# Performance work log

Hardware: AMD Instinct MI355X
Metric: run time of the kernel (lower is better)

The kernel has to match this reference:

```python
import jax, jax.numpy as jnp
import numpy as np

N = 50000
IN_DIM = 512
HID = 64
E = 800000


def setup_inputs() -> dict:
    key = jax.random.key(0)
    k1, k2, k3, k4 = jax.random.split(key, 4)
    x = jax.random.normal(k1, (N, IN_DIM), dtype=jnp.float32)
    edge_index = jax.random.randint(k2, (2, E), 0, N, dtype=jnp.int32)
    # Glorot-ish init for linear weights
    W1 = jax.random.normal(k3, (IN_DIM, HID), dtype=jnp.float32) / np.sqrt(IN_DIM)
    b1 = jnp.zeros((HID,), dtype=jnp.float32)
    W2 = jax.random.normal(k4, (HID, HID), dtype=jnp.float32) / np.sqrt(HID)
    b2 = jnp.zeros((HID,), dtype=jnp.float32)
    return {"x": x, "edge_index": edge_index, "W1": W1, "b1": b1, "W2": W2, "b2": b2}


def gcn_conv(x, src, dst, norm, W, b, n):
    # x' = D^{-1/2} (A+I) D^{-1/2} x W + b  (PyG GCNConv with self-loops)
    h = x @ W                                  # [N, out] dense GEMM
    msg = h[src] * norm[:, None]               # gather + scale per edge
    out = jax.ops.segment_sum(msg, dst, num_segments=n)  # scatter-add
    return out + b


def reference(x, edge_index, W1, b1, W2, b2):
    n = x.shape[0]
    loop = jnp.arange(n, dtype=edge_index.dtype)
    src = jnp.concatenate([edge_index[0], loop])  # add self-loops
    dst = jnp.concatenate([edge_index[1], loop])
    deg = jax.ops.segment_sum(jnp.ones_like(src, dtype=x.dtype), dst, num_segments=n)
    dinv = jnp.where(deg > 0, jax.lax.rsqrt(deg), 0.0)
    norm = dinv[src] * dinv[dst]               # symmetric normalization per edge
    h = gcn_conv(x, src, dst, norm, W1, b1, n)
    h = jax.nn.relu(h)
    # dropout is identity in eval mode (reference baseline)
    z = gcn_conv(h, src, dst, norm, W2, b2, n)
    return z
```

## Files before the change

kernel.cpp:

```cpp
#include <hip/hip_runtime.h>
#include <stdint.h>


typedef __attribute__((ext_vector_type(8))) short short8;
typedef __attribute__((ext_vector_type(4))) float f32x4;

#define SLOTS 64

__device__ __forceinline__ uint32_t bf16_rne(float f) {
  uint32_t u = __float_as_uint(f);
  return (u + 0x7FFFu + ((u >> 16) & 1u)) >> 16;
}

__global__ __launch_bounds__(256) void fill_wfrag_kernel(
    const int* __restrict__ src, const int* __restrict__ dst, int E,
    int* __restrict__ cursor, int* __restrict__ meta,
    const float* __restrict__ W1, const float* __restrict__ W2,
    short8* __restrict__ wh1, short8* __restrict__ wl1,
    short8* __restrict__ wh2, short8* __restrict__ wl2,
    int K1, int K2, int wblocks) {
  if ((int)blockIdx.x >= wblocks) {
    int i = (blockIdx.x - wblocks) * 256 + threadIdx.x;
    if (i < E) {
      int s = __builtin_nontemporal_load(src + i);
      int d = __builtin_nontemporal_load(dst + i);
      int pos = atomicAdd(&cursor[d], 1);
      if (pos < SLOTS) meta[(size_t)d * SLOTS + pos] = s;
    }
    return;
  }
  int idx = blockIdx.x * 256 + threadIdx.x;
  int tot1 = (K1 >> 5) * 256;
  int tot2 = (K2 >> 5) * 256;
  const float* W;
  short8 *wh, *wl;
  if (idx < tot1) {
    W = W1; wh = wh1; wl = wl1;
  } else if (idx < tot1 + tot2) {
    idx -= tot1;
    W = W2; wh = wh2; wl = wl2;
  } else {
    return;
  }
  int lane = idx & 63;
  int ct = (idx >> 6) & 3;
  int kt = idx >> 8;
  int m = lane & 15, q = lane >> 4;
  int col = ct * 16 + m;
  short8 h, l;
#pragma unroll
  for (int j = 0; j < 8; ++j) {
    float f = W[(size_t)(kt * 32 + q * 8 + j) * 64 + col];
    uint32_t hb = bf16_rne(f);
    float hf = __uint_as_float(hb << 16);
    float lo = f - hf;
    h[j] = (short)hb;
    l[j] = (short)bf16_rne(lo);
  }
  wh[idx] = h;
  wl[idx] = l;
}

__global__ __launch_bounds__(256) void gemm_mfma_kernel(
    const float* __restrict__ A, const short8* __restrict__ wh,
    const short8* __restrict__ wl, ushort* __restrict__ outb, int n, int K,
    int gblocks, const int* __restrict__ cursor, float* __restrict__ dinv,
    int ndinv) {
  if ((int)blockIdx.x >= gblocks) {
    int i = (blockIdx.x - gblocks) * 256 + threadIdx.x;
    if (i < ndinv) dinv[i] = rsqrtf((float)(cursor[i] + 1));
    return;
  }
  const int t = threadIdx.x;
  const int lane = t & 63;
  const int m = lane & 15, q = lane >> 4;
  const int row0 = blockIdx.x * 64 + (t >> 6) * 16;
  int r0 = row0 + m;
  if (r0 >= n) r0 = n - 1;
  const float* ap = A + (size_t)r0 * K + q * 8;
  const short8* whp = wh + lane;
  const short8* wlp = wl + lane;
  const int nkt = K >> 5;
  f32x4 acc[4];
#pragma unroll
  for (int c = 0; c < 4; ++c) acc[c] = 0.f;

  f32x4 xa0 = __builtin_nontemporal_load((const f32x4*)ap);
  f32x4 xa1 = __builtin_nontemporal_load((const f32x4*)(ap + 4));
  short8 bh[4] = {whp[0], whp[64], whp[128], whp[192]};
  short8 bl[4] = {wlp[0], wlp[64], wlp[128], wlp[192]};

  auto cvt = [&](const f32x4& u0, const f32x4& u1, short8& hi, short8& lo) {
    float xf[8] = {u0[0], u0[1], u0[2], u0[3], u1[0], u1[1], u1[2], u1[3]};
#pragma unroll
    for (int j = 0; j < 8; ++j) {
      uint32_t hb = bf16_rne(xf[j]);
      float hf = __uint_as_float(hb << 16);
      hi[j] = (short)hb;
      lo[j] = (short)bf16_rne(xf[j] - hf);
    }
  };
  auto compute = [&]() {
    short8 ah, al;
    cvt(xa0, xa1, ah, al);
#pragma unroll
    for (int c = 0; c < 4; ++c)
      acc[c] = __builtin_amdgcn_mfma_f32_16x16x32_bf16(ah, bh[c], acc[c], 0, 0, 0);
#pragma unroll
    for (int c = 0; c < 4; ++c)
      acc[c] = __builtin_amdgcn_mfma_f32_16x16x32_bf16(ah, bl[c], acc[c], 0, 0, 0);
#pragma unroll
    for (int c = 0; c < 4; ++c)
      acc[c] = __builtin_amdgcn_mfma_f32_16x16x32_bf16(al, bh[c], acc[c], 0, 0, 0);
  };

  for (int kt = 0; kt < nkt - 1; ++kt) {
    const float* an = ap + 32;
    f32x4 nxa0 = __builtin_nontemporal_load((const f32x4*)an);
    f32x4 nxa1 = __builtin_nontemporal_load((const f32x4*)(an + 4));
    const short8* whn = whp + 256;
    const short8* wln = wlp + 256;
    short8 nh[4] = {whn[0], whn[64], whn[128], whn[192]};
    short8 nl[4] = {wln[0], wln[64], wln[128], wln[192]};
    compute();
    xa0 = nxa0; xa1 = nxa1;
#pragma unroll
    for (int c = 0; c < 4; ++c) { bh[c] = nh[c]; bl[c] = nl[c]; }
    ap = an; whp = whn; wlp = wln;
  }
  compute();

#pragma unroll
  for (int i = 0; i < 4; ++i) {
    int rr = row0 + q * 4 + i;
    if (rr < n) {
      ushort* op = outb + (size_t)rr * 64 + m;
      op[0]  = (ushort)bf16_rne(acc[0][i]);
      op[16] = (ushort)bf16_rne(acc[1][i]);
      op[32] = (ushort)bf16_rne(acc[2][i]);
      op[48] = (ushort)bf16_rne(acc[3][i]);
    }
  }
}

__global__ __launch_bounds__(256) void agg_kernel(const ushort* __restrict__ H,
                                                  const int* __restrict__ deg,
                                                  const int* __restrict__ meta,
                                                  const float* __restrict__ dinv,
                                                  const float* __restrict__ bias,
                                                  float* __restrict__ out, int n,
                                                  int do_relu) {
  const int t = threadIdx.x;
  const int sl = t & 7;
  const int v = blockIdx.x * 32 + (t >> 3);
  if (v >= n) return;
  const float dv = dinv[v];
  const float dvv = dv * dv;
  float acc[8];
  {
    uint4 hv = *(const uint4*)&H[(size_t)v * 64 + (sl << 3)];
    uint32_t u[4] = {hv.x, hv.y, hv.z, hv.w};
#pragma unroll
    for (int j = 0; j < 4; ++j) {
      acc[2 * j]     = __uint_as_float(u[j] << 16) * dvv;
      acc[2 * j + 1] = __uint_as_float(u[j] & 0xFFFF0000u) * dvv;
    }
  }
  int dg = deg[v];
  if (dg > SLOTS) dg = SLOTS;
  int nc = (dg + 7) >> 3;
  const int4* p = (const int4*)(meta + (size_t)v * SLOTS);

  int4 ma0, ma1, mb0, mb1;
  uint4 ra[8], rb[8];
  float wa[8], wb[8];
  auto gath = [&](int4 c0, int4 c1, uint4* r, float* wr) {
    int u[8] = {c0.x, c0.y, c0.z, c0.w, c1.x, c1.y, c1.z, c1.w};
#pragma unroll
    for (int j = 0; j < 8; ++j) {
      unsigned idx = (unsigned)u[j];
      if (idx >= (unsigned)n) idx = 0;
      r[j] = *(const uint4*)&H[(size_t)idx * 64 + (sl << 3)];
      wr[j] = dinv[idx];
    }
  };
  auto consume = [&](int rem, const uint4* r, const float* wr) {
#pragma unroll
    for (int j = 0; j < 8; ++j) {
      const float wgt = (j < rem) ? wr[j] * dv : 0.f;
      uint32_t q[4] = {r[j].x, r[j].y, r[j].z, r[j].w};
#pragma unroll
      for (int k = 0; k < 4; ++k) {
        acc[2 * k]     = fmaf(__uint_as_float(q[k] << 16), wgt, acc[2 * k]);
        acc[2 * k + 1] = fmaf(__uint_as_float(q[k] & 0xFFFF0000u), wgt, acc[2 * k + 1]);
      }
    }
  };

  if (nc > 0) {
    ma0 = p[0]; ma1 = p[1];
    gath(ma0, ma1, ra, wa);
  }
  for (int c = 0; c < nc - 1; ++c) {
    mb0 = p[2 * c + 2]; mb1 = p[2 * c + 3];
    gath(mb0, mb1, rb, wb);
    consume(dg - (c << 3), ra, wa);
    ma0 = mb0; ma1 = mb1;
#pragma unroll
    for (int j = 0; j < 8; ++j) { ra[j] = rb[j]; wa[j] = wb[j]; }
  }
  if (nc > 0) consume(dg - ((nc - 1) << 3), ra, wa);

  const float4 blo = *(const float4*)&bias[sl << 3];
  const float4 bhi = *(const float4*)&bias[(sl << 3) + 4];
  float bb[8] = {blo.x, blo.y, blo.z, blo.w, bhi.x, bhi.y, bhi.z, bhi.w};
#pragma unroll
  for (int j = 0; j < 8; ++j) {
    acc[j] += bb[j];
    if (do_relu) acc[j] = fmaxf(acc[j], 0.f);
  }
  float* op = out + (size_t)v * 64 + (sl << 3);
  f32x4 v0 = {acc[0], acc[1], acc[2], acc[3]};
  f32x4 v1 = {acc[4], acc[5], acc[6], acc[7]};
  if (do_relu) {
    *(f32x4*)op = v0;
    *(f32x4*)(op + 4) = v1;
  } else {
    __builtin_nontemporal_store(v0, (f32x4*)op);
    __builtin_nontemporal_store(v1, (f32x4*)(op + 4));
  }
}

extern "C" void kernel_launch(void* const* d_in, const int* in_sizes, int n_in,
                              void* d_out, int out_size, void* d_ws, size_t ws_size,
                              hipStream_t stream) {
  const float* x = (const float*)d_in[0];
  const int* ei = (const int*)d_in[1];
  const float* W1 = (const float*)d_in[2];
  const float* b1 = (const float*)d_in[3];
  const float* W2 = (const float*)d_in[4];
  const float* b2 = (const float*)d_in[5];
  float* out = (float*)d_out;

  const int HID = in_sizes[3];
  const int IN_DIM = in_sizes[2] / HID;
  const int N = in_sizes[0] / IN_DIM;
  const int E = in_sizes[1] / 2;

  uint8_t* p = (uint8_t*)d_ws;
  auto alloc = [&](size_t bytes) {
    void* r = (void*)p;
    p += (bytes + 255) & ~(size_t)255;
    return r;
  };
  int* meta = (int*)alloc((size_t)N * SLOTS * 4);
  int* cursor = (int*)alloc((size_t)N * 4);
  float* dinv = (float*)alloc((size_t)N * 4);
  ushort* hb = (ushort*)alloc((size_t)N * HID * 2);
  float* h = (float*)alloc((size_t)N * HID * 4);
  short8* wh1 = (short8*)alloc((size_t)(IN_DIM >> 5) * 256 * 16);
  short8* wl1 = (short8*)alloc((size_t)(IN_DIM >> 5) * 256 * 16);
  short8* wh2 = (short8*)alloc((size_t)(HID >> 5) * 256 * 16);
  short8* wl2 = (short8*)alloc((size_t)(HID >> 5) * 256 * 16);

  const int* srcp = ei;
  const int* dstp = ei + E;

  (void)hipMemsetAsync(cursor, 0, (size_t)N * 4, stream);

  const int wtot = (IN_DIM >> 5) * 256 + (HID >> 5) * 256;
  const int wblocks = (wtot + 255) / 256;
  const int fblocks = (E + 255) / 256;
  fill_wfrag_kernel<<<wblocks + fblocks, 256, 0, stream>>>(
      srcp, dstp, E, cursor, meta, W1, W2, wh1, wl1, wh2, wl2, IN_DIM, HID, wblocks);

  const int g1 = (N + 63) / 64;
  const int dblk = (N + 255) / 256;
  gemm_mfma_kernel<<<g1 + dblk, 256, 0, stream>>>(x, wh1, wl1, hb, N, IN_DIM, g1,
                                                  cursor, dinv, N);
  agg_kernel<<<(N + 31) / 32, 256, 0, stream>>>(hb, cursor, meta, dinv, b1, h, N, 1);
  gemm_mfma_kernel<<<g1, 256, 0, stream>>>(h, wh2, wl2, hb, N, HID, g1,
                                           cursor, dinv, 0);
  agg_kernel<<<(N + 31) / 32, 256, 0, stream>>>(hb, cursor, meta, dinv, b2, out, N, 0);
}
```

Baseline: 283.6 us.

## Process two row tiles per wave in GEMM and use packed bf16 conversion

```diff
diff --git a/kernel.cpp b/kernel.cpp
--- a/kernel.cpp
+++ b/kernel.cpp
@@ -4,12 +4,19 @@
 
 typedef __attribute__((ext_vector_type(8))) short short8;
 typedef __attribute__((ext_vector_type(4))) float f32x4;
+typedef __attribute__((ext_vector_type(4))) unsigned int u32x4;
 
 #define SLOTS 64
 
 __device__ __forceinline__ uint32_t bf16_rne(float f) {
   uint32_t u = __float_as_uint(f);
   return (u + 0x7FFFu + ((u >> 16) & 1u)) >> 16;
+}
+
+__device__ __forceinline__ uint32_t cvt_pk_bf16(float a, float b) {
+  uint32_t r;
+  asm("v_cvt_pk_bf16_f32 %0, %1, %2" : "=v"(r) : "v"(a), "v"(b));
+  return r;
 }
 
 __global__ __launch_bounds__(256) void fill_wfrag_kernel(
@@ -74,73 +81,99 @@
   const int t = threadIdx.x;
   const int lane = t & 63;
   const int m = lane & 15, q = lane >> 4;
-  const int row0 = blockIdx.x * 64 + (t >> 6) * 16;
+  const int row0 = blockIdx.x * 128 + (t >> 6) * 32;
   int r0 = row0 + m;
+  int r1 = row0 + 16 + m;
   if (r0 >= n) r0 = n - 1;
-  const float* ap = A + (size_t)r0 * K + q * 8;
+  if (r1 >= n) r1 = n - 1;
+  const float* ap0 = A + (size_t)r0 * K + q * 8;
+  const float* ap1 = A + (size_t)r1 * K + q * 8;
   const short8* whp = wh + lane;
   const short8* wlp = wl + lane;
   const int nkt = K >> 5;
-  f32x4 acc[4];
-#pragma unroll
-  for (int c = 0; c < 4; ++c) acc[c] = 0.f;
-
-  f32x4 xa0 = __builtin_nontemporal_load((const f32x4*)ap);
-  f32x4 xa1 = __builtin_nontemporal_load((const f32x4*)(ap + 4));
+  f32x4 acc[2][4];
+#pragma unroll
+  for (int g = 0; g < 2; ++g)
+#pragma unroll
+    for (int c = 0; c < 4; ++c) acc[g][c] = 0.f;
+
+  f32x4 xa0 = *(const f32x4*)(ap0);
+  f32x4 xa1 = *(const f32x4*)(ap0 + 4);
+  f32x4 xb0 = *(const f32x4*)(ap1);
+  f32x4 xb1 = *(const f32x4*)(ap1 + 4);
   short8 bh[4] = {whp[0], whp[64], whp[128], whp[192]};
   short8 bl[4] = {wlp[0], wlp[64], wlp[128], wlp[192]};
 
   auto cvt = [&](const f32x4& u0, const f32x4& u1, short8& hi, short8& lo) {
-    float xf[8] = {u0[0], u0[1], u0[2], u0[3], u1[0], u1[1], u1[2], u1[3]};
-#pragma unroll
-    for (int j = 0; j < 8; ++j) {
-      uint32_t hb = bf16_rne(xf[j]);
-      float hf = __uint_as_float(hb << 16);
-      hi[j] = (short)hb;
-      lo[j] = (short)bf16_rne(xf[j] - hf);
-    }
+    u32x4 hw, lw;
+    hw[0] = cvt_pk_bf16(u0[0], u0[1]);
+    hw[1] = cvt_pk_bf16(u0[2], u0[3]);
+    hw[2] = cvt_pk_bf16(u1[0], u1[1]);
+    hw[3] = cvt_pk_bf16(u1[2], u1[3]);
+    lw[0] = cvt_pk_bf16(u0[0] - __uint_as_float(hw[0] << 16),
+                        u0[1] - __uint_as_float(hw[0] & 0xFFFF0000u));
+    lw[1] = cvt_pk_bf16(u0[2] - __uint_as_float(hw[1] << 16),
+                        u0[3] - __uint_as_float(hw[1] & 0xFFFF0000u));
+    lw[2] = cvt_pk_bf16(u1[0] - __uint_as_float(hw[2] << 16),
+                        u1[1] - __uint_as_float(hw[2] & 0xFFFF0000u));
+    lw[3] = cvt_pk_bf16(u1[2] - __uint_as_float(hw[3] << 16),
+                        u1[3] - __uint_as_float(hw[3] & 0xFFFF0000u));
+    hi = __builtin_bit_cast(short8, hw);
+    lo = __builtin_bit_cast(short8, lw);
   };
   auto compute = [&]() {
-    short8 ah, al;
-    cvt(xa0, xa1, ah, al);
-#pragma unroll
-    for (int c = 0; c < 4; ++c)
-      acc[c] = __builtin_amdgcn_mfma_f32_16x16x32_bf16(ah, bh[c], acc[c], 0, 0, 0);
-#pragma unroll
-    for (int c = 0; c < 4; ++c)
-      acc[c] = __builtin_amdgcn_mfma_f32_16x16x32_bf16(ah, bl[c], acc[c], 0, 0, 0);
-#pragma unroll
-    for (int c = 0; c < 4; ++c)
-      acc[c] = __builtin_amdgcn_mfma_f32_16x16x32_bf16(al, bh[c], acc[c], 0, 0, 0);
+    short8 ah0, al0, ah1, al1;
+    cvt(xa0, xa1, ah0, al0);
+    cvt(xb0, xb1, ah1, al1);
+#pragma unroll
+    for (int c = 0; c < 4; ++c) {
+      acc[0][c] = __builtin_amdgcn_mfma_f32_16x16x32_bf16(ah0, bh[c], acc[0][c], 0, 0, 0);
+      acc[1][c] = __builtin_amdgcn_mfma_f32_16x16x32_bf16(ah1, bh[c], acc[1][c], 0, 0, 0);
+    }
+#pragma unroll
+    for (int c = 0; c < 4; ++c) {
+      acc[0][c] = __builtin_amdgcn_mfma_f32_16x16x32_bf16(ah0, bl[c], acc[0][c], 0, 0, 0);
+      acc[1][c] = __builtin_amdgcn_mfma_f32_16x16x32_bf16(ah1, bl[c], acc[1][c], 0, 0, 0);
+    }
+#pragma unroll
+    for (int c = 0; c < 4; ++c) {
+      acc[0][c] = __builtin_amdgcn_mfma_f32_16x16x32_bf16(al0, bh[c], acc[0][c], 0, 0, 0);
+      acc[1][c] = __builtin_amdgcn_mfma_f32_16x16x32_bf16(al1, bh[c], acc[1][c], 0, 0, 0);
+    }
   };
 
   for (int kt = 0; kt < nkt - 1; ++kt) {
-    const float* an = ap + 32;
-    f32x4 nxa0 = __builtin_nontemporal_load((const f32x4*)an);
-    f32x4 nxa1 = __builtin_nontemporal_load((const f32x4*)(an + 4));
+    const float* an0 = ap0 + 32;
+    const float* an1 = ap1 + 32;
+    f32x4 nxa0 = *(const f32x4*)(an0);
+    f32x4 nxa1 = *(const f32x4*)(an0 + 4);
+    f32x4 nxb0 = *(const f32x4*)(an1);
+    f32x4 nxb1 = *(const f32x4*)(an1 + 4);
     const short8* whn = whp + 256;
     const short8* wln = wlp + 256;
     short8 nh[4] = {whn[0], whn[64], whn[128], whn[192]};
     short8 nl[4] = {wln[0], wln[64], wln[128], wln[192]};
     compute();
-    xa0 = nxa0; xa1 = nxa1;
+    xa0 = nxa0; xa1 = nxa1; xb0 = nxb0; xb1 = nxb1;
 #pragma unroll
     for (int c = 0; c < 4; ++c) { bh[c] = nh[c]; bl[c] = nl[c]; }
-    ap = an; whp = whn; wlp = wln;
+    ap0 = an0; ap1 = an1; whp = whn; wlp = wln;
   }
   compute();
 
 #pragma unroll
-  for (int i = 0; i < 4; ++i) {
-    int rr = row0 + q * 4 + i;
-    if (rr < n) {
-      ushort* op = outb + (size_t)rr * 64 + m;
-      op[0]  = (ushort)bf16_rne(acc[0][i]);
-      op[16] = (ushort)bf16_rne(acc[1][i]);
-      op[32] = (ushort)bf16_rne(acc[2][i]);
-      op[48] = (ushort)bf16_rne(acc[3][i]);
-    }
-  }
+  for (int g = 0; g < 2; ++g)
+#pragma unroll
+    for (int i = 0; i < 4; ++i) {
+      int rr = row0 + g * 16 + q * 4 + i;
+      if (rr < n) {
+        ushort* op = outb + (size_t)rr * 64 + m;
+        op[0]  = (ushort)bf16_rne(acc[g][0][i]);
+        op[16] = (ushort)bf16_rne(acc[g][1][i]);
+        op[32] = (ushort)bf16_rne(acc[g][2][i]);
+        op[48] = (ushort)bf16_rne(acc[g][3][i]);
+      }
+    }
 }
 
 __global__ __launch_bounds__(256) void agg_kernel(const ushort* __restrict__ H,
@@ -274,7 +307,7 @@
   fill_wfrag_kernel<<<wblocks + fblocks, 256, 0, stream>>>(
       srcp, dstp, E, cursor, meta, W1, W2, wh1, wl1, wh2, wl2, IN_DIM, HID, wblocks);
 
-  const int g1 = (N + 63) / 64;
+  const int g1 = (N + 127) / 128;
   const int dblk = (N + 255) / 256;
   gemm_mfma_kernel<<<g1 + dblk, 256, 0, stream>>>(x, wh1, wl1, hb, N, IN_DIM, g1,
                                                   cursor, dinv, N);
```

Result: faster. 267.4 us (-5.7%).
